# Kernel optimization log

Measured on AMD Instinct MI355X. Metric: run time of the kernel, lower is better.

Reference implementation:

```python
import jax, jax.numpy as jnp
import numpy as np

SIGMA_BOOST = 2.0   # sparse-hyper util.SIGMA_BOOST
EPSILON = 1e-6      # sparse-hyper util.EPSILON (10e-7)
B, N = 512, 16384   # batch, size


def setup_inputs() -> dict:
    key = jax.random.key(0)
    k1, k2, k3, k4, k5 = jax.random.split(key, 5)
    return {
        "x": jax.random.normal(k1, (B, N), jnp.float32),
        "noise": jax.random.normal(k2, (B, N, 2), jnp.float32),
        "pmeans": jax.random.normal(k3, (N, 2), jnp.float32),
        "psigmas": jax.random.normal(k4, (N,), jnp.float32),
        "pvalues": jax.random.normal(k5, (N,), jnp.float32),
    }


def reference(x, noise, pmeans, psigmas, pvalues):
    b, n = x.shape
    s = jnp.float32(n)  # square size (n, n); both dims equal
    # hyper(): transform_means = sigmoid * (size-1); transform_sigmas = (softplus(.+boost)+eps) * size
    means = jax.nn.sigmoid(pmeans)[None] * (s - 1.0)                    # (1, n, 2) -> bcast (b, n, 2)
    sigmas = (jax.nn.softplus(psigmas + SIGMA_BOOST) + EPSILON)[None, :, None] * s  # (1, n, 1)
    # Normal(means, sigmas).sample() -- non-differentiable sample
    samples = jax.lax.stop_gradient(means + sigmas * noise)             # (b, n, 2)
    # round, clamp to [0, n-1]
    indices = jnp.clip(jnp.round(samples).astype(jnp.int32), 0, n - 1)  # (b, n, 2)
    rows, cols = indices[..., 0], indices[..., 1]                       # (b, n) each
    values = jnp.broadcast_to(pvalues[None, :], (b, n))
    # sparse.contract: y[b, rows[b,t]] += values[b,t] * x[b, cols[b,t]]
    contrib = values * jnp.take_along_axis(x, cols, axis=1)             # (b, n)
    y = jnp.zeros((b, n), x.dtype).at[jnp.arange(b)[:, None], rows].add(contrib)
    return y
```

## Files before the change

kernel.cpp:

```cpp
#include <hip/hip_runtime.h>
#include <math.h>

#define SIGMA_BOOST 2.0f
#define EPSILON 1e-6f

__device__ __forceinline__ float4 compute_param(const float2* __restrict__ pmeans,
                                                const float* __restrict__ psigmas,
                                                const float* __restrict__ pvalues,
                                                int t, int N) {
    float2 pm = pmeans[t];
    float scale = (float)(N - 1);
    float m0 = __fmul_rn(__fdiv_rn(1.0f, __fadd_rn(1.0f, expf(-pm.x))), scale);
    float m1 = __fmul_rn(__fdiv_rn(1.0f, __fadd_rn(1.0f, expf(-pm.y))), scale);
    float z  = __fadd_rn(psigmas[t], SIGMA_BOOST);
    float sp = __fadd_rn(fmaxf(z, 0.0f), log1pf(expf(-fabsf(z))));
    float sg = __fmul_rn(__fadd_rn(sp, EPSILON), (float)N);
    return make_float4(m0, m1, sg, pvalues[t]);
}

__global__ void params_kernel(const float2* __restrict__ pmeans,
                              const float* __restrict__ psigmas,
                              const float* __restrict__ pvalues,
                              float4* __restrict__ params, int N) {
    int t = blockIdx.x * blockDim.x + threadIdx.x;
    if (t < N) params[t] = compute_param(pmeans, psigmas, pvalues, t, N);
}

template <bool STAGED, bool INLINE_PARAMS, int UNROLL>
__launch_bounds__(1024, 1)
__global__ void contract_kernel(const float* __restrict__ x,
                                const float2* __restrict__ noise,
                                const float4* __restrict__ params,
                                const float2* __restrict__ pmeans,
                                const float* __restrict__ psigmas,
                                const float* __restrict__ pvalues,
                                float* __restrict__ y, int N) {
    extern __shared__ float lds[];
    float* ly = lds;
    float* lx = STAGED ? (lds + N) : nullptr;

    const int b = blockIdx.x;
    const int tid = threadIdx.x;
    const int nthr = blockDim.x;
    const int n4 = N >> 2;

    const float* xb = x + (size_t)b * N;
    float4* ly4 = (float4*)ly;
    const float4* xb4 = (const float4*)xb;

    if (STAGED) {
        float4* lx4 = (float4*)lx;
        for (int i = tid; i < n4; i += nthr) {
            ly4[i] = make_float4(0.f, 0.f, 0.f, 0.f);
            lx4[i] = xb4[i];
        }
    } else {
        for (int i = tid; i < n4; i += nthr)
            ly4[i] = make_float4(0.f, 0.f, 0.f, 0.f);
    }
    __syncthreads();

    const float4* nb4 = (const float4*)(noise + (size_t)b * N);
    const float fN1 = (float)(N - 1);

    for (int t0 = tid * UNROLL; t0 < N; t0 += nthr * UNROLL) {
        float nz[2 * UNROLL];
#pragma unroll
        for (int u = 0; u < UNROLL / 2; ++u) {
            float4 nv = nb4[(t0 >> 1) + u];
            nz[4 * u + 0] = nv.x; nz[4 * u + 1] = nv.y;
            nz[4 * u + 2] = nv.z; nz[4 * u + 3] = nv.w;
        }
        float4 p[UNROLL];
#pragma unroll
        for (int u = 0; u < UNROLL; ++u)
            p[u] = INLINE_PARAMS ? compute_param(pmeans, psigmas, pvalues, t0 + u, N)
                                 : params[t0 + u];
        int r[UNROLL], c[UNROLL];
#pragma unroll
        for (int u = 0; u < UNROLL; ++u) {
            float s0 = __fadd_rn(p[u].x, __fmul_rn(p[u].z, nz[2 * u + 0]));
            float s1 = __fadd_rn(p[u].y, __fmul_rn(p[u].z, nz[2 * u + 1]));
            r[u] = (int)fminf(fmaxf(rintf(s0), 0.0f), fN1);
            c[u] = (int)fminf(fmaxf(rintf(s1), 0.0f), fN1);
        }
        float xv[UNROLL];
#pragma unroll
        for (int u = 0; u < UNROLL; ++u)
            xv[u] = STAGED ? lx[c[u]] : xb[c[u]];
#pragma unroll
        for (int u = 0; u < UNROLL; ++u)
            atomicAdd(&ly[r[u]], __fmul_rn(p[u].w, xv[u]));
    }
    __syncthreads();

    float4* yb4 = (float4*)(y + (size_t)b * N);
    for (int i = tid; i < n4; i += nthr) yb4[i] = ly4[i];
}

extern "C" void kernel_launch(void* const* d_in, const int* in_sizes, int n_in,
                              void* d_out, int out_size, void* d_ws, size_t ws_size,
                              hipStream_t stream) {
    const float*  x       = (const float*)d_in[0];
    const float2* noise   = (const float2*)d_in[1];
    const float2* pmeans  = (const float2*)d_in[2];
    const float*  psigmas = (const float*)d_in[3];
    const float*  pvalues = (const float*)d_in[4];
    float* y = (float*)d_out;

    const int N = in_sizes[3];
    const int B = in_sizes[0] / N;

    const size_t params_bytes = (size_t)N * sizeof(float4);
    const bool use_ws = (ws_size >= params_bytes) && (d_ws != nullptr);

    const int block = 1024;
    const size_t staged_lds = 2 * (size_t)N * sizeof(float);
    const size_t acc_lds    = (size_t)N * sizeof(float);

    int dev = 0;
    (void)hipGetDevice(&dev);
    int max_lds = 0;
    (void)hipDeviceGetAttribute(&max_lds, hipDeviceAttributeMaxSharedMemoryPerBlock, dev);
    const bool staged = (size_t)max_lds >= staged_lds;

    float4* params = (float4*)d_ws;
    if (use_ws)
        params_kernel<<<(N + 255) / 256, 256, 0, stream>>>(pmeans, psigmas, pvalues, params, N);

    if (staged) {
        if (use_ws) {
            (void)hipFuncSetAttribute(
                reinterpret_cast<const void*>(&contract_kernel<true, false, 4>),
                hipFuncAttributeMaxDynamicSharedMemorySize, (int)staged_lds);
            contract_kernel<true, false, 4><<<B, block, staged_lds, stream>>>(
                x, noise, params, nullptr, nullptr, nullptr, y, N);
        } else {
            (void)hipFuncSetAttribute(
                reinterpret_cast<const void*>(&contract_kernel<true, true, 4>),
                hipFuncAttributeMaxDynamicSharedMemorySize, (int)staged_lds);
            contract_kernel<true, true, 4><<<B, block, staged_lds, stream>>>(
                x, noise, nullptr, pmeans, psigmas, pvalues, y, N);
        }
    } else {
        if (use_ws) {
            contract_kernel<false, false, 8><<<B, block, acc_lds, stream>>>(
                x, noise, params, nullptr, nullptr, nullptr, y, N);
        } else {
            contract_kernel<false, true, 8><<<B, block, acc_lds, stream>>>(
                x, noise, nullptr, pmeans, psigmas, pvalues, y, N);
        }
    }
}
```

Before: 168.2 us.

## Add fully unrolled contract kernel that prefetches noise and params before staging

Adds a specialized contract kernel for N equal to 16384, where each thread owns a fixed set of 16 elements. It issues all noise and parameter global loads into registers before staging x and zeroing the LDS accumulator, so that latency overlaps with the staging loop. Loads are arranged so each float4 of noise pairs with two param entries, and the launch-bounds hint is raised. This uses many more registers per thread and only applies to this exact size.

```diff
diff --git a/kernel.cpp b/kernel.cpp
--- a/kernel.cpp
+++ b/kernel.cpp
@@ -26,6 +26,69 @@
     if (t < N) params[t] = compute_param(pmeans, psigmas, pvalues, t, N);
 }
 
+template <int U4>
+__launch_bounds__(1024, 4)
+__global__ void contract_fast(const float* __restrict__ x,
+                              const float4* __restrict__ noise4,
+                              const float4* __restrict__ params,
+                              float* __restrict__ y, int N) {
+    extern __shared__ float lds[];
+    float* ly = lds;
+    float* lx = lds + N;
+    const int b = blockIdx.x;
+    const int tid = threadIdx.x;
+    const int nthr = 1024;
+    const int n4 = N >> 2;
+
+    const float4* nb4 = noise4 + (size_t)b * (size_t)(N >> 1);
+
+    float4 nv[U4], pa[U4], pb[U4];
+#pragma unroll
+    for (int u = 0; u < U4; ++u) {
+        int j = tid + u * nthr;
+        nv[u] = nb4[j];
+        pa[u] = params[2 * j];
+        pb[u] = params[2 * j + 1];
+    }
+
+    const float4* xb4 = (const float4*)(x + (size_t)b * N);
+    float4* lx4 = (float4*)lx;
+    float4* ly4 = (float4*)ly;
+#pragma unroll
+    for (int i = tid; i < n4; i += nthr) {
+        lx4[i] = xb4[i];
+        ly4[i] = make_float4(0.f, 0.f, 0.f, 0.f);
+    }
+    __syncthreads();
+
+    const float fN1 = (float)(N - 1);
+    int r[2 * U4], c[2 * U4];
+    float pv[2 * U4];
+#pragma unroll
+    for (int u = 0; u < U4; ++u) {
+        float s0 = __fadd_rn(pa[u].x, __fmul_rn(pa[u].z, nv[u].x));
+        float s1 = __fadd_rn(pa[u].y, __fmul_rn(pa[u].z, nv[u].y));
+        r[2 * u] = (int)fminf(fmaxf(rintf(s0), 0.f), fN1);
+        c[2 * u] = (int)fminf(fmaxf(rintf(s1), 0.f), fN1);
+        pv[2 * u] = pa[u].w;
+        float s2 = __fadd_rn(pb[u].x, __fmul_rn(pb[u].z, nv[u].z));
+        float s3 = __fadd_rn(pb[u].y, __fmul_rn(pb[u].z, nv[u].w));
+        r[2 * u + 1] = (int)fminf(fmaxf(rintf(s2), 0.f), fN1);
+        c[2 * u + 1] = (int)fminf(fmaxf(rintf(s3), 0.f), fN1);
+        pv[2 * u + 1] = pb[u].w;
+    }
+    float xv[2 * U4];
+#pragma unroll
+    for (int k = 0; k < 2 * U4; ++k) xv[k] = lx[c[k]];
+#pragma unroll
+    for (int k = 0; k < 2 * U4; ++k) atomicAdd(&ly[r[k]], __fmul_rn(pv[k], xv[k]));
+    __syncthreads();
+
+    float4* yb4 = (float4*)(y + (size_t)b * N);
+#pragma unroll
+    for (int i = tid; i < n4; i += nthr) yb4[i] = ly4[i];
+}
+
 template <bool STAGED, bool INLINE_PARAMS, int UNROLL>
 __launch_bounds__(1024, 1)
 __global__ void contract_kernel(const float* __restrict__ x,
@@ -67,9 +130,9 @@
         float nz[2 * UNROLL];
 #pragma unroll
         for (int u = 0; u < UNROLL / 2; ++u) {
-            float4 nv = nb4[(t0 >> 1) + u];
-            nz[4 * u + 0] = nv.x; nz[4 * u + 1] = nv.y;
-            nz[4 * u + 2] = nv.z; nz[4 * u + 3] = nv.w;
+            float4 nvv = nb4[(t0 >> 1) + u];
+            nz[4 * u + 0] = nvv.x; nz[4 * u + 1] = nvv.y;
+            nz[4 * u + 2] = nvv.z; nz[4 * u + 3] = nvv.w;
         }
         float4 p[UNROLL];
 #pragma unroll
@@ -84,13 +147,13 @@
             r[u] = (int)fminf(fmaxf(rintf(s0), 0.0f), fN1);
             c[u] = (int)fminf(fmaxf(rintf(s1), 0.0f), fN1);
         }
-        float xv[UNROLL];
+        float xvv[UNROLL];
 #pragma unroll
         for (int u = 0; u < UNROLL; ++u)
-            xv[u] = STAGED ? lx[c[u]] : xb[c[u]];
+            xvv[u] = STAGED ? lx[c[u]] : xb[c[u]];
 #pragma unroll
         for (int u = 0; u < UNROLL; ++u)
-            atomicAdd(&ly[r[u]], __fmul_rn(p[u].w, xv[u]));
+            atomicAdd(&ly[r[u]], __fmul_rn(p[u].w, xvv[u]));
     }
     __syncthreads();
 
@@ -128,7 +191,14 @@
     if (use_ws)
         params_kernel<<<(N + 255) / 256, 256, 0, stream>>>(pmeans, psigmas, pvalues, params, N);
 
-    if (staged) {
+    constexpr int U4 = 8;
+    if (staged && use_ws && N == 2 * 1024 * U4) {
+        (void)hipFuncSetAttribute(
+            reinterpret_cast<const void*>(&contract_fast<U4>),
+            hipFuncAttributeMaxDynamicSharedMemorySize, (int)staged_lds);
+        contract_fast<U4><<<B, block, staged_lds, stream>>>(
+            x, (const float4*)noise, params, y, N);
+    } else if (staged) {
         if (use_ws) {
             (void)hipFuncSetAttribute(
                 reinterpret_cast<const void*>(&contract_kernel<true, false, 4>),
```

Measured after the change: 186.6 us. 1.11x slower.
